# Optimization experiments

Measured on AMD Instinct MI355X. Metric: run time of the kernel, lower is better.

Reference implementation:

```python
import jax, jax.numpy as jnp
import numpy as np

N_NODES = 50000
N_EDGES = 800000
D = 128
N_GRAPHS = 64


def setup_inputs() -> dict:
    key = jax.random.key(0)
    ks = jax.random.split(key, 10)
    x = jax.random.normal(ks[0], (N_NODES, D), dtype=jnp.float32)
    edge_weight = jax.random.uniform(ks[1], (N_EDGES,), dtype=jnp.float32)
    W1 = jax.random.normal(ks[2], (D, D), dtype=jnp.float32) / np.sqrt(D)
    b1 = jax.random.normal(ks[3], (D,), dtype=jnp.float32) * 0.01
    W2 = jax.random.normal(ks[4], (D, D), dtype=jnp.float32) / np.sqrt(D)
    b2 = jax.random.normal(ks[5], (D,), dtype=jnp.float32) * 0.01
    Wh = jax.random.normal(ks[6], (D, 1), dtype=jnp.float32) / np.sqrt(D)
    bh = jax.random.normal(ks[7], (1,), dtype=jnp.float32) * 0.01
    edge_index = jax.random.randint(ks[8], (2, N_EDGES), 0, N_NODES, dtype=jnp.int64)
    batch = jnp.sort(jax.random.randint(ks[9], (N_NODES,), 0, N_GRAPHS, dtype=jnp.int64))
    return {"x": x, "edge_weight": edge_weight, "W1": W1, "b1": b1,
            "W2": W2, "b2": b2, "Wh": Wh, "bh": bh,
            "edge_index": edge_index, "batch": batch}


def reference(x, edge_weight, W1, b1, W2, b2, Wh, bh, edge_index, batch):
    N = x.shape[0]
    # --- GCN normalization with self-loops (computed once; shared by layers) ---
    row, col = edge_index[0], edge_index[1]
    loop = jnp.arange(N, dtype=edge_index.dtype)
    row2 = jnp.concatenate([row, loop])   # source nodes
    col2 = jnp.concatenate([col, loop])   # target nodes
    ew2 = jnp.concatenate([edge_weight, jnp.ones((N,), dtype=x.dtype)])
    deg = jax.ops.segment_sum(ew2, col2, num_segments=N)
    dinv = jnp.where(deg > 0, jax.lax.rsqrt(deg), 0.0)
    norm = dinv[row2] * ew2 * dinv[col2]  # [E+N]

    def gcn_conv(h, W, b):
        h = h @ W                                   # [N, D_out]
        msg = norm[:, None] * h[row2]               # gather + scale, [E+N, D_out]
        return jax.ops.segment_sum(msg, col2, num_segments=N) + b

    # dropout is identity in eval mode
    h = jax.nn.relu(gcn_conv(x, W1, b1))
    h = jax.nn.relu(gcn_conv(h, W2, b2))

    # --- global mean pool over graphs ---
    counts = jax.ops.segment_sum(jnp.ones((N,), dtype=h.dtype), batch, num_segments=N_GRAPHS)
    pooled = jax.ops.segment_sum(h, batch, num_segments=N_GRAPHS)
    pooled = pooled / jnp.maximum(counts, 1.0)[:, None]
    return pooled @ Wh + bh
```

## Files before the change

kernel.cpp:

```cpp
#include <hip/hip_runtime.h>
#include <hip/hip_bf16.h>
#include <hip/hip_fp16.h>
#include <hip/hip_fp8.h>

#define N_NODES  50000
#define N_EDGES  800000
#define D        128
#define N_GRAPHS 64
#define CAP      64
#define EW_SCALE 1048576.0f
#define NB_GEMM1 391
#define NPART    196
#define PCAP     5120
#define EPB      4096
#define NB_SCAT  196
#define NB_AGG16 3125
#define NB_HEAD  6250

typedef _Float16 half8 __attribute__((ext_vector_type(8)));
typedef _Float16 half4 __attribute__((ext_vector_type(4)));
typedef float   float4v __attribute__((ext_vector_type(4)));
typedef float   f32x2   __attribute__((ext_vector_type(2)));

__device__ __forceinline__ float hu2f(unsigned short u) {
    __half_raw hr; hr.x = u;
    return __half2float(__half(hr));
}
__device__ __forceinline__ unsigned char f32_fp8(float f) {
    __hip_fp8_e4m3 q(f);
    return (unsigned char)q.__x;
}
__device__ __forceinline__ void unpack_pd(unsigned long long p, int& n, float& dv) {
    int c = (int)(p >> 40);
    n = c < CAP ? c : CAP;
    dv = rsqrtf(1.0f + (float)(p & 0xFFFFFFFFFFULL) * (1.0f / EW_SCALE));
}

__global__ __launch_bounds__(512) void scatter_gemm1_kernel(const int* __restrict__ ei,
                                                            const float* __restrict__ ew,
                                                            unsigned long long* __restrict__ staging,
                                                            unsigned int* __restrict__ partCnt,
                                                            const float* __restrict__ X,
                                                            const float* __restrict__ W,
                                                            unsigned char* __restrict__ Y8) {
    extern __shared__ char smem[];
    const int tid = threadIdx.x;

    if (blockIdx.x < NB_SCAT) {
        unsigned long long* pay = (unsigned long long*)smem;
        unsigned int* dest  = (unsigned int*)(smem + 32768);
        unsigned int* hist  = (unsigned int*)(smem + 49152);
        unsigned int* pref  = (unsigned int*)(smem + 50176);
        unsigned int* gbase = (unsigned int*)(smem + 51200);
        unsigned int* cur   = (unsigned int*)(smem + 52224);

        const int e0 = blockIdx.x * EPB;
        for (int p = tid; p < NPART; p += 512) hist[p] = 0;
        __syncthreads();

        int rs[8], cs[8]; float wsv[8];
#pragma unroll
        for (int k = 0; k < 8; k++) {
            int e = e0 + k * 512 + tid;
            if (e < N_EDGES) {
                rs[k] = ei[e];
                cs[k] = ei[N_EDGES + e];
                wsv[k] = ew[e];
                atomicAdd(&hist[cs[k] >> 8], 1u);
            } else cs[k] = -1;
        }
        __syncthreads();

        if (tid < NPART) pref[tid] = hist[tid];
        __syncthreads();
        for (int off = 1; off < NPART; off <<= 1) {
            unsigned v = 0;
            if (tid < NPART && tid >= off) v = pref[tid - off];
            __syncthreads();
            if (tid < NPART) pref[tid] += v;
            __syncthreads();
        }
        if (tid < NPART) {
            unsigned excl = pref[tid] - hist[tid];
            gbase[tid] = atomicAdd(&partCnt[tid], hist[tid]);
            cur[tid]  = excl;
            pref[tid] = excl;
        }
        __syncthreads();

#pragma unroll
        for (int k = 0; k < 8; k++) {
            if (cs[k] >= 0) {
                int p = cs[k] >> 8;
                unsigned r = atomicAdd(&cur[p], 1u);
                unsigned lo = (unsigned)rs[k] | ((unsigned)cs[k] << 16);
                pay[r]  = (unsigned long long)lo |
                          ((unsigned long long)__float_as_uint(wsv[k]) << 32);
                unsigned loff = gbase[p] + (r - pref[p]);
                dest[r] = (loff < PCAP) ? (unsigned)(p * PCAP + loff) : 0xFFFFFFFFu;
            }
        }
        __syncthreads();

        const int total = (e0 + EPB <= N_EDGES) ? EPB : (N_EDGES - e0);
        for (int j = tid; j < total; j += 512)
            if (dest[j] != 0xFFFFFFFFu)
                staging[dest[j]] = pay[j];
        return;
    }

    _Float16 (*Xs)[72] = (_Float16(*)[72])smem;
    _Float16 (*Wt)[72] = (_Float16(*)[72])(smem + 128 * 72 * 2);
    const int row0 = (blockIdx.x - NB_SCAT) * 128;
    const int wv   = tid >> 6;
    const int lane = tid & 63;
    const int quad = lane >> 4;
    const int l16  = lane & 15;

    float4v acc[8] = {};
    for (int kt = 0; kt < 4; kt++) {
        const int kbase = kt * 32;
        {
            int r  = tid >> 2;
            int rr = row0 + r; if (rr >= N_NODES) rr = N_NODES - 1;
            int k0 = (tid & 3) * 8;
            const float4* src = (const float4*)(X + (size_t)rr * 128 + kbase + k0);
#pragma unroll
            for (int i = 0; i < 2; i++) {
                float4 v = src[i];
                half4 hv;
                hv[0] = (_Float16)v.x; hv[1] = (_Float16)v.y;
                hv[2] = (_Float16)v.z; hv[3] = (_Float16)v.w;
                *(half4*)(&Xs[r][k0 + i * 4]) = hv;
            }
        }
        {
            int k  = tid >> 4;
            int c0 = (tid & 15) * 8;
            const float4* src = (const float4*)(W + (size_t)(kbase + k) * 128 + c0);
#pragma unroll
            for (int i = 0; i < 2; i++) {
                float4 v = src[i];
                Wt[c0 + i * 4 + 0][k] = (_Float16)v.x;
                Wt[c0 + i * 4 + 1][k] = (_Float16)v.y;
                Wt[c0 + i * 4 + 2][k] = (_Float16)v.z;
                Wt[c0 + i * 4 + 3][k] = (_Float16)v.w;
            }
        }
        __syncthreads();

        half8 b0 = *(const half8*)(&Wt[wv * 16 + l16][quad * 8]);
#pragma unroll
        for (int rt = 0; rt < 8; rt++) {
            half8 a = *(const half8*)(&Xs[rt * 16 + l16][quad * 8]);
            acc[rt] = __builtin_amdgcn_mfma_f32_16x16x32_f16(a, b0, acc[rt], 0, 0, 0);
        }
        __syncthreads();
    }
#pragma unroll
    for (int rt = 0; rt < 8; rt++)
#pragma unroll
        for (int r = 0; r < 4; r++) {
            int row = row0 + rt * 16 + quad * 4 + r;
            if (row < N_NODES)
                Y8[(size_t)row * 128 + wv * 16 + l16] = f32_fp8(acc[rt][r]);
        }
}

__global__ __launch_bounds__(512) void bucket_kernel(const unsigned long long* __restrict__ staging,
                                                     const unsigned int* __restrict__ partCnt,
                                                     unsigned int* __restrict__ bucket,
                                                     unsigned long long* __restrict__ packed) {
    extern __shared__ char smem[];
    unsigned int* img  = (unsigned int*)smem;
    unsigned int* cnt  = (unsigned int*)(smem + 65536);
    unsigned int* udeg = (unsigned int*)(smem + 66560);
    const int tid = threadIdx.x;
    const int p = blockIdx.x;
    for (int i = tid; i < 256; i += 512) { cnt[i] = 0; udeg[i] = 0; }
    __syncthreads();

    int n = (int)partCnt[p];
    if (n > PCAP) n = PCAP;
    const unsigned long long* src = staging + (size_t)p * PCAP;
    for (int j = tid; j < n; j += 512) {
        unsigned long long e = src[j];
        unsigned lo = (unsigned)e;
        int r  = lo & 0xFFFF;
        int dl = (lo >> 16) & 255;
        float w = __uint_as_float((unsigned)(e >> 32));
        atomicAdd(&udeg[dl], (unsigned)(w * EW_SCALE + 0.5f));
        unsigned slot = atomicAdd(&cnt[dl], 1u);
        if (slot < CAP) {
            unsigned short wh = __half_as_ushort(__float2half_rn(w));
            img[dl * CAP + slot] = (unsigned)r | ((unsigned)wh << 16);
        }
    }
    __syncthreads();

    const int dst0 = p * 256;
    for (int i = tid; i < 256 * CAP; i += 512) {
        int dst = dst0 + (i >> 6);
        if (dst < N_NODES)
            bucket[(size_t)dst * CAP + (i & 63)] = img[i];
    }
    for (int dl = tid; dl < 256; dl += 512) {
        int dst = dst0 + dl;
        if (dst < N_NODES)
            packed[dst] = ((unsigned long long)cnt[dl] << 40)
                        | (unsigned long long)udeg[dl];
    }
}

__global__ __launch_bounds__(512) void agg1_gemm2_kernel(const unsigned char* __restrict__ x8in,
                                                         const unsigned long long* __restrict__ packed,
                                                         const unsigned int* __restrict__ bucket,
                                                         const float* __restrict__ b1,
                                                         const float* __restrict__ W2,
                                                         unsigned char* __restrict__ x2) {
    __shared__ _Float16 sh1[16][136];
    const int wv   = threadIdx.x >> 6;
    const int lane = threadIdx.x & 63;
    const int g    = lane >> 4;
    const int fl   = lane & 15;
    const int node0 = blockIdx.x * 16;

    const int nodeA = node0 + wv * 2;
    const int nodeB = nodeA + 1;
    int nA; float dvA; unpack_pd(packed[nodeA], nA, dvA);
    int nB; float dvB; unpack_pd(packed[nodeB], nB, dvB);

    unsigned pkA = 0u, pkB = 0u;
    if (lane < nA) {
        unsigned eh = __builtin_nontemporal_load(&bucket[(size_t)nodeA * CAP + lane]);
        int src = eh & 0xFFFFu;
        int sn; float sdv; unpack_pd(packed[src], sn, sdv);
        float v = hu2f((unsigned short)(eh >> 16)) * sdv;
        pkA = (unsigned)src | ((unsigned)__half_as_ushort(__float2half_rn(v)) << 16);
    }
    if (lane < nB) {
        unsigned eh = __builtin_nontemporal_load(&bucket[(size_t)nodeB * CAP + lane]);
        int src = eh & 0xFFFFu;
        int sn; float sdv; unpack_pd(packed[src], sn, sdv);
        float v = hu2f((unsigned short)(eh >> 16)) * sdv;
        pkB = (unsigned)src | ((unsigned)__half_as_ushort(__float2half_rn(v)) << 16);
    }
    int pkiA = (int)pkA, pkiB = (int)pkB;
    int nmax = nA > nB ? nA : nB;

    const unsigned char* base = x8in + fl * 8;

    float aA[8] = {}, aB[8] = {};
    for (int i = 0; i < nmax; i += 8) {
        unsigned hA0 = (unsigned)__shfl(pkiA, i + g);
        unsigned hA1 = (unsigned)__shfl(pkiA, i + 4 + g);
        unsigned hB0 = (unsigned)__shfl(pkiB, i + g);
        unsigned hB1 = (unsigned)__shfl(pkiB, i + 4 + g);
        uint2 dA0 = *(const uint2*)(base + (size_t)(hA0 & 0xFFFFu) * 128);
        uint2 dA1 = *(const uint2*)(base + (size_t)(hA1 & 0xFFFFu) * 128);
        uint2 dB0 = *(const uint2*)(base + (size_t)(hB0 & 0xFFFFu) * 128);
        uint2 dB1 = *(const uint2*)(base + (size_t)(hB1 & 0xFFFFu) * 128);
        float vA0 = hu2f((unsigned short)(hA0 >> 16));
        float vA1 = hu2f((unsigned short)(hA1 >> 16));
        float vB0 = hu2f((unsigned short)(hB0 >> 16));
        float vB1 = hu2f((unsigned short)(hB1 >> 16));
#pragma unroll
        for (int d = 0; d < 2; d++) {
            unsigned wA0 = d ? dA0.y : dA0.x;
            unsigned wA1 = d ? dA1.y : dA1.x;
            unsigned wB0 = d ? dB0.y : dB0.x;
            unsigned wB1 = d ? dB1.y : dB1.x;
            f32x2 A0lo = __builtin_amdgcn_cvt_pk_f32_fp8((int)wA0, false);
            f32x2 A0hi = __builtin_amdgcn_cvt_pk_f32_fp8((int)wA0, true);
            f32x2 A1lo = __builtin_amdgcn_cvt_pk_f32_fp8((int)wA1, false);
            f32x2 A1hi = __builtin_amdgcn_cvt_pk_f32_fp8((int)wA1, true);
            f32x2 B0lo = __builtin_amdgcn_cvt_pk_f32_fp8((int)wB0, false);
            f32x2 B0hi = __builtin_amdgcn_cvt_pk_f32_fp8((int)wB0, true);
            f32x2 B1lo = __builtin_amdgcn_cvt_pk_f32_fp8((int)wB1, false);
            f32x2 B1hi = __builtin_amdgcn_cvt_pk_f32_fp8((int)wB1, true);
            aA[d*4+0] += vA0 * A0lo[0] + vA1 * A1lo[0];
            aA[d*4+1] += vA0 * A0lo[1] + vA1 * A1lo[1];
            aA[d*4+2] += vA0 * A0hi[0] + vA1 * A1hi[0];
            aA[d*4+3] += vA0 * A0hi[1] + vA1 * A1hi[1];
            aB[d*4+0] += vB0 * B0lo[0] + vB1 * B1lo[0];
            aB[d*4+1] += vB0 * B0lo[1] + vB1 * B1lo[1];
            aB[d*4+2] += vB0 * B0hi[0] + vB1 * B1hi[0];
            aB[d*4+3] += vB0 * B0hi[1] + vB1 * B1hi[1];
        }
    }

#pragma unroll
    for (int k = 0; k < 8; k++) {
        aA[k] += __shfl_xor(aA[k], 16, 64);
        aA[k] += __shfl_xor(aA[k], 32, 64);
        aB[k] += __shfl_xor(aB[k], 16, 64);
        aB[k] += __shfl_xor(aB[k], 32, 64);
    }

    {
        uint2 dsA = *(const uint2*)(base + (size_t)nodeA * 128);
        uint2 dsB = *(const uint2*)(base + (size_t)nodeB * 128);
#pragma unroll
        for (int d = 0; d < 2; d++) {
            unsigned wA = d ? dsA.y : dsA.x;
            unsigned wB = d ? dsB.y : dsB.x;
            f32x2 Alo = __builtin_amdgcn_cvt_pk_f32_fp8((int)wA, false);
            f32x2 Ahi = __builtin_amdgcn_cvt_pk_f32_fp8((int)wA, true);
            f32x2 Blo = __builtin_amdgcn_cvt_pk_f32_fp8((int)wB, false);
            f32x2 Bhi = __builtin_amdgcn_cvt_pk_f32_fp8((int)wB, true);
            aA[d*4+0] += dvA * Alo[0]; aA[d*4+1] += dvA * Alo[1];
            aA[d*4+2] += dvA * Ahi[0]; aA[d*4+3] += dvA * Ahi[1];
            aB[d*4+0] += dvB * Blo[0]; aB[d*4+1] += dvB * Blo[1];
            aB[d*4+2] += dvB * Bhi[0]; aB[d*4+3] += dvB * Bhi[1];
        }
    }

    if (g == 0) {
        float4 bb0 = ((const float4*)b1)[fl * 2];
        float4 bb1 = ((const float4*)b1)[fl * 2 + 1];
        float bb[8] = {bb0.x, bb0.y, bb0.z, bb0.w, bb1.x, bb1.y, bb1.z, bb1.w};
        half8 hvA, hvB;
#pragma unroll
        for (int k = 0; k < 8; k++) {
            hvA[k] = (_Float16)fmaxf(dvA * aA[k] + bb[k], 0.0f);
            hvB[k] = (_Float16)fmaxf(dvB * aB[k] + bb[k], 0.0f);
        }
        *(half8*)(&sh1[wv * 2][fl * 8])     = hvA;
        *(half8*)(&sh1[wv * 2 + 1][fl * 8]) = hvB;
    }
    __syncthreads();

    const int quad = lane >> 4;
    const int l16  = lane & 15;
    float4v acc0 = {};
#pragma unroll
    for (int kc = 0; kc < 4; kc++) {
        const int k0 = kc * 32;
        half8 a = *(const half8*)(&sh1[l16][k0 + quad * 8]);
        const float* wp = W2 + (size_t)(k0 + quad * 8) * 128 + wv * 16 + l16;
        half8 b;
#pragma unroll
        for (int jj = 0; jj < 8; jj++) b[jj] = (_Float16)wp[jj * 128];
        acc0 = __builtin_amdgcn_mfma_f32_16x16x32_f16(a, b, acc0, 0, 0, 0);
    }
#pragma unroll
    for (int r = 0; r < 4; r++) {
        int row = node0 + quad * 4 + r;
        int rn; float s;
        unpack_pd(packed[row], rn, s);
        x2[(size_t)row * 128 + wv * 16 + l16] = f32_fp8(acc0[r] * s);
    }
}

__global__ __launch_bounds__(256) void agg_head_kernel(const unsigned char* __restrict__ x8,
                                                       const unsigned long long* __restrict__ packed,
                                                       const unsigned int* __restrict__ bucket,
                                                       const float* __restrict__ bias,
                                                       const float* __restrict__ Wh,
                                                       float* __restrict__ nodedot) {
    const int wv   = threadIdx.x >> 6;
    const int lane = threadIdx.x & 63;
    const int g    = lane >> 4;
    const int fl   = lane & 15;

    const int nodeA = blockIdx.x * 8 + wv * 2;
    const int nodeB = nodeA + 1;
    int nA; float dvA; unpack_pd(packed[nodeA], nA, dvA);
    int nB; float dvB; unpack_pd(packed[nodeB], nB, dvB);

    unsigned ehA = (lane < nA) ? __builtin_nontemporal_load(&bucket[(size_t)nodeA * CAP + lane]) : 0u;
    unsigned ehB = (lane < nB) ? __builtin_nontemporal_load(&bucket[(size_t)nodeB * CAP + lane]) : 0u;
    int eiA = (int)ehA, eiB = (int)ehB;
    int nmax = nA > nB ? nA : nB;

    const unsigned char* base = x8 + fl * 8;

    float aA[8] = {}, aB[8] = {};
    for (int i = 0; i < nmax; i += 8) {
        unsigned hA0 = (unsigned)__shfl(eiA, i + g);
        unsigned hA1 = (unsigned)__shfl(eiA, i + 4 + g);
        unsigned hB0 = (unsigned)__shfl(eiB, i + g);
        unsigned hB1 = (unsigned)__shfl(eiB, i + 4 + g);
        uint2 dA0 = *(const uint2*)(base + (size_t)(hA0 & 0xFFFFu) * 128);
        uint2 dA1 = *(const uint2*)(base + (size_t)(hA1 & 0xFFFFu) * 128);
        uint2 dB0 = *(const uint2*)(base + (size_t)(hB0 & 0xFFFFu) * 128);
        uint2 dB1 = *(const uint2*)(base + (size_t)(hB1 & 0xFFFFu) * 128);
        float vA0 = hu2f((unsigned short)(hA0 >> 16));
        float vA1 = hu2f((unsigned short)(hA1 >> 16));
        float vB0 = hu2f((unsigned short)(hB0 >> 16));
        float vB1 = hu2f((unsigned short)(hB1 >> 16));
#pragma unroll
        for (int d = 0; d < 2; d++) {
            unsigned wA0 = d ? dA0.y : dA0.x;
            unsigned wA1 = d ? dA1.y : dA1.x;
            unsigned wB0 = d ? dB0.y : dB0.x;
            unsigned wB1 = d ? dB1.y : dB1.x;
            f32x2 A0lo = __builtin_amdgcn_cvt_pk_f32_fp8((int)wA0, false);
            f32x2 A0hi = __builtin_amdgcn_cvt_pk_f32_fp8((int)wA0, true);
            f32x2 A1lo = __builtin_amdgcn_cvt_pk_f32_fp8((int)wA1, false);
            f32x2 A1hi = __builtin_amdgcn_cvt_pk_f32_fp8((int)wA1, true);
            f32x2 B0lo = __builtin_amdgcn_cvt_pk_f32_fp8((int)wB0, false);
            f32x2 B0hi = __builtin_amdgcn_cvt_pk_f32_fp8((int)wB0, true);
            f32x2 B1lo = __builtin_amdgcn_cvt_pk_f32_fp8((int)wB1, false);
            f32x2 B1hi = __builtin_amdgcn_cvt_pk_f32_fp8((int)wB1, true);
            aA[d*4+0] += vA0 * A0lo[0] + vA1 * A1lo[0];
            aA[d*4+1] += vA0 * A0lo[1] + vA1 * A1lo[1];
            aA[d*4+2] += vA0 * A0hi[0] + vA1 * A1hi[0];
            aA[d*4+3] += vA0 * A0hi[1] + vA1 * A1hi[1];
            aB[d*4+0] += vB0 * B0lo[0] + vB1 * B1lo[0];
            aB[d*4+1] += vB0 * B0lo[1] + vB1 * B1lo[1];
            aB[d*4+2] += vB0 * B0hi[0] + vB1 * B1hi[0];
            aB[d*4+3] += vB0 * B0hi[1] + vB1 * B1hi[1];
        }
    }

#pragma unroll
    for (int k = 0; k < 8; k++) {
        aA[k] += __shfl_xor(aA[k], 16, 64);
        aA[k] += __shfl_xor(aA[k], 32, 64);
        aB[k] += __shfl_xor(aB[k], 16, 64);
        aB[k] += __shfl_xor(aB[k], 32, 64);
    }

    {
        uint2 dsA = *(const uint2*)(base + (size_t)nodeA * 128);
        uint2 dsB = *(const uint2*)(base + (size_t)nodeB * 128);
#pragma unroll
        for (int d = 0; d < 2; d++) {
            unsigned wA = d ? dsA.y : dsA.x;
            unsigned wB = d ? dsB.y : dsB.x;
            f32x2 Alo = __builtin_amdgcn_cvt_pk_f32_fp8((int)wA, false);
            f32x2 Ahi = __builtin_amdgcn_cvt_pk_f32_fp8((int)wA, true);
            f32x2 Blo = __builtin_amdgcn_cvt_pk_f32_fp8((int)wB, false);
            f32x2 Bhi = __builtin_amdgcn_cvt_pk_f32_fp8((int)wB, true);
            aA[d*4+0] += Alo[0]; aA[d*4+1] += Alo[1];
            aA[d*4+2] += Ahi[0]; aA[d*4+3] += Ahi[1];
            aB[d*4+0] += Blo[0]; aB[d*4+1] += Blo[1];
            aB[d*4+2] += Bhi[0]; aB[d*4+3] += Bhi[1];
        }
    }

    float4 bb0 = ((const float4*)bias)[fl * 2];
    float4 bb1 = ((const float4*)bias)[fl * 2 + 1];
    float4 wh0 = ((const float4*)Wh)[fl * 2];
    float4 wh1 = ((const float4*)Wh)[fl * 2 + 1];
    float bb[8] = {bb0.x, bb0.y, bb0.z, bb0.w, bb1.x, bb1.y, bb1.z, bb1.w};
    float ww[8] = {wh0.x, wh0.y, wh0.z, wh0.w, wh1.x, wh1.y, wh1.z, wh1.w};
    float sA = 0.0f, sB = 0.0f;
#pragma unroll
    for (int k = 0; k < 8; k++) {
        sA += fmaxf(dvA * aA[k] + bb[k], 0.0f) * ww[k];
        sB += fmaxf(dvB * aB[k] + bb[k], 0.0f) * ww[k];
    }
#pragma unroll
    for (int off = 8; off > 0; off >>= 1) {
        sA += __shfl_xor(sA, off, 64);
        sB += __shfl_xor(sB, off, 64);
    }
    if (lane == 0) {
        nodedot[nodeA] = sA;
        nodedot[nodeB] = sB;
    }
}

__global__ __launch_bounds__(256) void final2_kernel(const float* __restrict__ nodedot,
                                                     const int* __restrict__ batch,
                                                     const float* __restrict__ bh,
                                                     float* __restrict__ out) {
    __shared__ float red[256];
    int g = blockIdx.x;
    int lo = 0, hi = N_NODES;
    while (lo < hi) { int mid = (lo + hi) >> 1; if (batch[mid] < g) lo = mid + 1; else hi = mid; }
    int a = lo;
    hi = N_NODES;
    while (lo < hi) { int mid = (lo + hi) >> 1; if (batch[mid] < g + 1) lo = mid + 1; else hi = mid; }
    int b = lo;

    float s = 0.0f;
    for (int n = a + threadIdx.x; n < b; n += 256) s += nodedot[n];
    red[threadIdx.x] = s;
    __syncthreads();
#pragma unroll
    for (int off = 128; off > 0; off >>= 1) {
        if (threadIdx.x < off) red[threadIdx.x] += red[threadIdx.x + off];
        __syncthreads();
    }
    if (threadIdx.x == 0)
        out[g] = red[0] / fmaxf((float)(b - a), 1.0f) + bh[0];
}

extern "C" void kernel_launch(void* const* d_in, const int* in_sizes, int n_in,
                              void* d_out, int out_size, void* d_ws, size_t ws_size,
                              hipStream_t stream) {
    const float* x   = (const float*)d_in[0];
    const float* ew  = (const float*)d_in[1];
    const float* W1  = (const float*)d_in[2];
    const float* b1  = (const float*)d_in[3];
    const float* W2  = (const float*)d_in[4];
    const float* b2  = (const float*)d_in[5];
    const float* Wh  = (const float*)d_in[6];
    const float* bh  = (const float*)d_in[7];
    const int*   ei  = (const int*)d_in[8];
    const int*   bat = (const int*)d_in[9];
    float* out = (float*)d_out;

    char* ws = (char*)d_ws;
    unsigned char* bufA8 = (unsigned char*)ws;            ws += (size_t)N_NODES * D;
    unsigned char* bufB8 = (unsigned char*)ws;            ws += (size_t)N_NODES * D;
    ws += 128 - ((size_t)ws & 127);
    unsigned int* bucket = (unsigned int*)ws;             ws += (size_t)N_NODES * CAP * 4;
    unsigned long long* packed = (unsigned long long*)ws; ws += (size_t)N_NODES * 8;
    unsigned long long* staging = (unsigned long long*)ws; ws += (size_t)NPART * PCAP * 8;
    float* nodedot = (float*)ws;                          ws += (size_t)N_NODES * 4;
    unsigned int* partCnt = (unsigned int*)ws;            ws += 1024;

    hipMemsetAsync(partCnt, 0, 1024, stream);

    scatter_gemm1_kernel<<<NB_SCAT + NB_GEMM1, 512, 53248, stream>>>(
        ei, ew, staging, partCnt, x, W1, bufA8);

    bucket_kernel<<<NPART, 512, 67584, stream>>>(staging, partCnt, bucket, packed);

    agg1_gemm2_kernel<<<NB_AGG16, 512, 0, stream>>>(bufA8, packed, bucket, b1, W2, bufB8);

    agg_head_kernel<<<NB_HEAD, 256, 0, stream>>>(bufB8, packed, bucket, b2, Wh, nodedot);

    final2_kernel<<<N_GRAPHS, 256, 0, stream>>>(nodedot, bat, bh, out);
}
```

Before: 186.2 us.

## Sort nodes by in-degree so aggregation waves process similar-degree node pairs

Builds a per-node degree histogram and rank in the bucket kernel, then a new perm kernel runs a prefix scan and emits a permutation of nodes grouped by in-degree. Both aggregation kernels pick nodes through this permutation, so each wave's two nodes (and each block's sixteen) have matching degrees. This is meant to cut divergence from the shared nmax loop. In exchange it adds a kernel launch, global atomics on a 65-entry histogram, and scattered non-contiguous node accesses and output writes.

```diff
diff --git a/kernel.cpp b/kernel.cpp
--- a/kernel.cpp
+++ b/kernel.cpp
@@ -16,6 +16,7 @@
 #define NB_SCAT  196
 #define NB_AGG16 3125
 #define NB_HEAD  6250
+#define NB_PERM  196
 
 typedef _Float16 half8 __attribute__((ext_vector_type(8)));
 typedef _Float16 half4 __attribute__((ext_vector_type(4)));
@@ -170,14 +171,20 @@
 __global__ __launch_bounds__(512) void bucket_kernel(const unsigned long long* __restrict__ staging,
                                                      const unsigned int* __restrict__ partCnt,
                                                      unsigned int* __restrict__ bucket,
-                                                     unsigned long long* __restrict__ packed) {
+                                                     unsigned long long* __restrict__ packed,
+                                                     unsigned int* __restrict__ rank,
+                                                     unsigned int* __restrict__ degHist) {
     extern __shared__ char smem[];
-    unsigned int* img  = (unsigned int*)smem;
-    unsigned int* cnt  = (unsigned int*)(smem + 65536);
-    unsigned int* udeg = (unsigned int*)(smem + 66560);
+    unsigned int* img    = (unsigned int*)smem;
+    unsigned int* cnt    = (unsigned int*)(smem + 65536);
+    unsigned int* udeg   = (unsigned int*)(smem + 66560);
+    unsigned int* hist65 = (unsigned int*)(smem + 67584);
+    unsigned int* base65 = (unsigned int*)(smem + 68096);
+    unsigned int* lrank  = (unsigned int*)(smem + 68608);
     const int tid = threadIdx.x;
     const int p = blockIdx.x;
     for (int i = tid; i < 256; i += 512) { cnt[i] = 0; udeg[i] = 0; }
+    for (int i = tid; i < 65; i += 512) hist65[i] = 0;
     __syncthreads();
 
     int n = (int)partCnt[p];
@@ -199,6 +206,18 @@
     __syncthreads();
 
     const int dst0 = p * 256;
+    if (tid < 256 && dst0 + tid < N_NODES) {
+        int deg = cnt[tid] < CAP ? cnt[tid] : CAP;
+        lrank[tid] = atomicAdd(&hist65[deg], 1u);
+    }
+    __syncthreads();
+    if (tid < 65) base65[tid] = atomicAdd(&degHist[tid], hist65[tid]);
+    __syncthreads();
+    if (tid < 256 && dst0 + tid < N_NODES) {
+        int deg = cnt[tid] < CAP ? cnt[tid] : CAP;
+        rank[dst0 + tid] = base65[deg] + lrank[tid];
+    }
+
     for (int i = tid; i < 256 * CAP; i += 512) {
         int dst = dst0 + (i >> 6);
         if (dst < N_NODES)
@@ -212,21 +231,52 @@
     }
 }
 
+__global__ __launch_bounds__(256) void perm_kernel(const unsigned long long* __restrict__ packed,
+                                                   const unsigned int* __restrict__ rank,
+                                                   const unsigned int* __restrict__ degHist,
+                                                   unsigned int* __restrict__ perm) {
+    __shared__ unsigned int bb[65];
+    __shared__ unsigned int ex[65];
+    const int tid = threadIdx.x;
+    if (tid < 65) bb[tid] = degHist[tid];
+    __syncthreads();
+    for (int off = 1; off < 65; off <<= 1) {
+        unsigned v = 0;
+        if (tid < 65 && tid >= off) v = bb[tid - off];
+        __syncthreads();
+        if (tid < 65) bb[tid] += v;
+        __syncthreads();
+    }
+    if (tid < 65) ex[tid] = bb[tid] - degHist[tid];
+    __syncthreads();
+    int n = blockIdx.x * 256 + tid;
+    if (n < N_NODES) {
+        int deg = (int)(packed[n] >> 40);
+        if (deg > CAP) deg = CAP;
+        perm[ex[deg] + rank[n]] = (unsigned)n;
+    }
+}
+
 __global__ __launch_bounds__(512) void agg1_gemm2_kernel(const unsigned char* __restrict__ x8in,
                                                          const unsigned long long* __restrict__ packed,
                                                          const unsigned int* __restrict__ bucket,
+                                                         const unsigned int* __restrict__ perm,
                                                          const float* __restrict__ b1,
                                                          const float* __restrict__ W2,
                                                          unsigned char* __restrict__ x2) {
     __shared__ _Float16 sh1[16][136];
+    __shared__ unsigned int pnode[16];
     const int wv   = threadIdx.x >> 6;
     const int lane = threadIdx.x & 63;
     const int g    = lane >> 4;
     const int fl   = lane & 15;
     const int node0 = blockIdx.x * 16;
 
-    const int nodeA = node0 + wv * 2;
-    const int nodeB = nodeA + 1;
+    if (threadIdx.x < 16) pnode[threadIdx.x] = perm[node0 + threadIdx.x];
+    __syncthreads();
+
+    const int nodeA = pnode[wv * 2];
+    const int nodeB = pnode[wv * 2 + 1];
     int nA; float dvA; unpack_pd(packed[nodeA], nA, dvA);
     int nB; float dvB; unpack_pd(packed[nodeB], nB, dvB);
 
@@ -345,7 +395,7 @@
     }
 #pragma unroll
     for (int r = 0; r < 4; r++) {
-        int row = node0 + quad * 4 + r;
+        int row = pnode[quad * 4 + r];
         int rn; float s;
         unpack_pd(packed[row], rn, s);
         x2[(size_t)row * 128 + wv * 16 + l16] = f32_fp8(acc0[r] * s);
@@ -355,6 +405,7 @@
 __global__ __launch_bounds__(256) void agg_head_kernel(const unsigned char* __restrict__ x8,
                                                        const unsigned long long* __restrict__ packed,
                                                        const unsigned int* __restrict__ bucket,
+                                                       const unsigned int* __restrict__ perm,
                                                        const float* __restrict__ bias,
                                                        const float* __restrict__ Wh,
                                                        float* __restrict__ nodedot) {
@@ -363,8 +414,9 @@
     const int g    = lane >> 4;
     const int fl   = lane & 15;
 
-    const int nodeA = blockIdx.x * 8 + wv * 2;
-    const int nodeB = nodeA + 1;
+    const int idxA = blockIdx.x * 8 + wv * 2;
+    const int nodeA = (int)perm[idxA];
+    const int nodeB = (int)perm[idxA + 1];
     int nA; float dvA; unpack_pd(packed[nodeA], nA, dvA);
     int nB; float dvB; unpack_pd(packed[nodeB], nB, dvB);
 
@@ -512,18 +564,27 @@
     unsigned long long* packed = (unsigned long long*)ws; ws += (size_t)N_NODES * 8;
     unsigned long long* staging = (unsigned long long*)ws; ws += (size_t)NPART * PCAP * 8;
     float* nodedot = (float*)ws;                          ws += (size_t)N_NODES * 4;
-    unsigned int* partCnt = (unsigned int*)ws;            ws += 1024;
-
-    hipMemsetAsync(partCnt, 0, 1024, stream);
+    unsigned int* rank = (unsigned int*)ws;               ws += (size_t)N_NODES * 4;
+    unsigned int* perm = (unsigned int*)ws;               ws += (size_t)N_NODES * 4;
+    char* ctrl = ws;                                      ws += 2048;
+    unsigned int* partCnt = (unsigned int*)ctrl;
+    unsigned int* degHist = (unsigned int*)(ctrl + 1024);
+
+    hipMemsetAsync(ctrl, 0, 2048, stream);
 
     scatter_gemm1_kernel<<<NB_SCAT + NB_GEMM1, 512, 53248, stream>>>(
         ei, ew, staging, partCnt, x, W1, bufA8);
 
-    bucket_kernel<<<NPART, 512, 67584, stream>>>(staging, partCnt, bucket, packed);
-
-    agg1_gemm2_kernel<<<NB_AGG16, 512, 0, stream>>>(bufA8, packed, bucket, b1, W2, bufB8);
-
-    agg_head_kernel<<<NB_HEAD, 256, 0, stream>>>(bufB8, packed, bucket, b2, Wh, nodedot);
+    bucket_kernel<<<NPART, 512, 69632, stream>>>(staging, partCnt, bucket, packed,
+                                                 rank, degHist);
+
+    perm_kernel<<<NB_PERM, 256, 0, stream>>>(packed, rank, degHist, perm);
+
+    agg1_gemm2_kernel<<<NB_AGG16, 512, 0, stream>>>(bufA8, packed, bucket, perm,
+                                                    b1, W2, bufB8);
+
+    agg_head_kernel<<<NB_HEAD, 256, 0, stream>>>(bufB8, packed, bucket, perm,
+                                                 b2, Wh, nodedot);
 
     final2_kernel<<<N_GRAPHS, 256, 0, stream>>>(nodedot, bat, bh, out);
 }
```

New measurement: 197.0 us. +5.8%, slower.

## Pre-scale layer-1 features by source dinv before fp8 quantization

Applied to the files above, without the earlier changes.

GEMM1 now writes fp16 output. The bucket kernel then multiplies each node's row by its own rsqrt degree and quantizes it to fp8. Because of this, the first aggregation kernel no longer loads packed[src] per edge or recomputes rsqrt to scale edge weights, and the self-loop term drops its dinv multiply. This removes a dependent random gather and some ALU work from the latency-bound aggregation. In exchange it adds an extra fp16 write/read pass over the node features, and the fp16 buffer is aliased over the later fp8 output buffer.

```diff
diff --git a/kernel.cpp b/kernel.cpp
--- a/kernel.cpp
+++ b/kernel.cpp
@@ -42,7 +42,7 @@
                                                             unsigned int* __restrict__ partCnt,
                                                             const float* __restrict__ X,
                                                             const float* __restrict__ W,
-                                                            unsigned char* __restrict__ Y8) {
+                                                            _Float16* __restrict__ Y16) {
     extern __shared__ char smem[];
     const int tid = threadIdx.x;
 
@@ -163,14 +163,16 @@
         for (int r = 0; r < 4; r++) {
             int row = row0 + rt * 16 + quad * 4 + r;
             if (row < N_NODES)
-                Y8[(size_t)row * 128 + wv * 16 + l16] = f32_fp8(acc[rt][r]);
+                Y16[(size_t)row * 128 + wv * 16 + l16] = (_Float16)acc[rt][r];
         }
 }
 
 __global__ __launch_bounds__(512) void bucket_kernel(const unsigned long long* __restrict__ staging,
                                                      const unsigned int* __restrict__ partCnt,
                                                      unsigned int* __restrict__ bucket,
-                                                     unsigned long long* __restrict__ packed) {
+                                                     unsigned long long* __restrict__ packed,
+                                                     const _Float16* __restrict__ X16,
+                                                     unsigned char* __restrict__ X8) {
     extern __shared__ char smem[];
     unsigned int* img  = (unsigned int*)smem;
     unsigned int* cnt  = (unsigned int*)(smem + 65536);
@@ -210,6 +212,26 @@
             packed[dst] = ((unsigned long long)cnt[dl] << 40)
                         | (unsigned long long)udeg[dl];
     }
+
+    for (int i = tid; i < 256 * 16; i += 512) {
+        int dl  = i >> 4;
+        int seg = i & 15;
+        int dst = dst0 + dl;
+        if (dst < N_NODES) {
+            float dv = rsqrtf(1.0f + (float)udeg[dl] * (1.0f / EW_SCALE));
+            half8 hv = *(const half8*)(X16 + (size_t)dst * 128 + seg * 8);
+            uint2 q;
+            q.x = (unsigned)f32_fp8((float)hv[0] * dv)
+                | ((unsigned)f32_fp8((float)hv[1] * dv) << 8)
+                | ((unsigned)f32_fp8((float)hv[2] * dv) << 16)
+                | ((unsigned)f32_fp8((float)hv[3] * dv) << 24);
+            q.y = (unsigned)f32_fp8((float)hv[4] * dv)
+                | ((unsigned)f32_fp8((float)hv[5] * dv) << 8)
+                | ((unsigned)f32_fp8((float)hv[6] * dv) << 16)
+                | ((unsigned)f32_fp8((float)hv[7] * dv) << 24);
+            *(uint2*)(X8 + (size_t)dst * 128 + seg * 8) = q;
+        }
+    }
 }
 
 __global__ __launch_bounds__(512) void agg1_gemm2_kernel(const unsigned char* __restrict__ x8in,
@@ -230,22 +252,9 @@
     int nA; float dvA; unpack_pd(packed[nodeA], nA, dvA);
     int nB; float dvB; unpack_pd(packed[nodeB], nB, dvB);
 
-    unsigned pkA = 0u, pkB = 0u;
-    if (lane < nA) {
-        unsigned eh = __builtin_nontemporal_load(&bucket[(size_t)nodeA * CAP + lane]);
-        int src = eh & 0xFFFFu;
-        int sn; float sdv; unpack_pd(packed[src], sn, sdv);
-        float v = hu2f((unsigned short)(eh >> 16)) * sdv;
-        pkA = (unsigned)src | ((unsigned)__half_as_ushort(__float2half_rn(v)) << 16);
-    }
-    if (lane < nB) {
-        unsigned eh = __builtin_nontemporal_load(&bucket[(size_t)nodeB * CAP + lane]);
-        int src = eh & 0xFFFFu;
-        int sn; float sdv; unpack_pd(packed[src], sn, sdv);
-        float v = hu2f((unsigned short)(eh >> 16)) * sdv;
-        pkB = (unsigned)src | ((unsigned)__half_as_ushort(__float2half_rn(v)) << 16);
-    }
-    int pkiA = (int)pkA, pkiB = (int)pkB;
+    unsigned ehA = (lane < nA) ? __builtin_nontemporal_load(&bucket[(size_t)nodeA * CAP + lane]) : 0u;
+    unsigned ehB = (lane < nB) ? __builtin_nontemporal_load(&bucket[(size_t)nodeB * CAP + lane]) : 0u;
+    int pkiA = (int)ehA, pkiB = (int)ehB;
     int nmax = nA > nB ? nA : nB;
 
     const unsigned char* base = x8in + fl * 8;
@@ -308,10 +317,10 @@
             f32x2 Ahi = __builtin_amdgcn_cvt_pk_f32_fp8((int)wA, true);
             f32x2 Blo = __builtin_amdgcn_cvt_pk_f32_fp8((int)wB, false);
             f32x2 Bhi = __builtin_amdgcn_cvt_pk_f32_fp8((int)wB, true);
-            aA[d*4+0] += dvA * Alo[0]; aA[d*4+1] += dvA * Alo[1];
-            aA[d*4+2] += dvA * Ahi[0]; aA[d*4+3] += dvA * Ahi[1];
-            aB[d*4+0] += dvB * Blo[0]; aB[d*4+1] += dvB * Blo[1];
-            aB[d*4+2] += dvB * Bhi[0]; aB[d*4+3] += dvB * Bhi[1];
+            aA[d*4+0] += Alo[0]; aA[d*4+1] += Alo[1];
+            aA[d*4+2] += Ahi[0]; aA[d*4+3] += Ahi[1];
+            aB[d*4+0] += Blo[0]; aB[d*4+1] += Blo[1];
+            aB[d*4+2] += Bhi[0]; aB[d*4+3] += Bhi[1];
         }
     }
 
@@ -506,7 +515,8 @@
 
     char* ws = (char*)d_ws;
     unsigned char* bufA8 = (unsigned char*)ws;            ws += (size_t)N_NODES * D;
-    unsigned char* bufB8 = (unsigned char*)ws;            ws += (size_t)N_NODES * D;
+    _Float16* bufA16 = (_Float16*)ws;
+    unsigned char* bufB8 = (unsigned char*)ws;            ws += (size_t)N_NODES * D * 2;
     ws += 128 - ((size_t)ws & 127);
     unsigned int* bucket = (unsigned int*)ws;             ws += (size_t)N_NODES * CAP * 4;
     unsigned long long* packed = (unsigned long long*)ws; ws += (size_t)N_NODES * 8;
@@ -517,9 +527,10 @@
     hipMemsetAsync(partCnt, 0, 1024, stream);
 
     scatter_gemm1_kernel<<<NB_SCAT + NB_GEMM1, 512, 53248, stream>>>(
-        ei, ew, staging, partCnt, x, W1, bufA8);
-
-    bucket_kernel<<<NPART, 512, 67584, stream>>>(staging, partCnt, bucket, packed);
+        ei, ew, staging, partCnt, x, W1, bufA16);
+
+    bucket_kernel<<<NPART, 512, 67584, stream>>>(staging, partCnt, bucket, packed,
+                                                 bufA16, bufA8);
 
     agg1_gemm2_kernel<<<NB_AGG16, 512, 0, stream>>>(bufA8, packed, bucket, b1, W2, bufB8);
 
```

After: 186.3 us. Within noise of the previous version (+0.1%).
